# Kernel optimization log

Measured on AMD Instinct MI355X. Metric: run time of the kernel, lower is better.

The kernel has to match this reference:

```python
import jax, jax.numpy as jnp
import numpy as np

N_HEAD = 16
N_EMBD = 1024


def setup_inputs() -> dict:
    key = jax.random.key(0)
    k1, k2, k3 = jax.random.split(key, 3)
    B, T = 2, 2048
    x = jax.random.normal(k1, (B, T, N_EMBD), dtype=jnp.float32)
    w_attn = jax.random.normal(k2, (N_EMBD, 3 * N_EMBD), dtype=jnp.float32) * 0.02
    b_attn = jnp.zeros((3 * N_EMBD,), dtype=jnp.float32)
    w_proj = jax.random.normal(k3, (N_EMBD, N_EMBD), dtype=jnp.float32) * 0.02
    b_proj = jnp.zeros((N_EMBD,), dtype=jnp.float32)
    return {"x": x, "w_attn": w_attn, "b_attn": b_attn, "w_proj": w_proj, "b_proj": b_proj}


def _split_heads(t):
    # [B, T, E] -> [B, H, T, hd]
    B, T, E = t.shape
    return t.reshape(B, T, N_HEAD, E // N_HEAD).transpose(0, 2, 1, 3)


def reference(x, w_attn, b_attn, w_proj, b_proj):
    B, T, E = x.shape
    hd = E // N_HEAD
    c = x @ w_attn + b_attn                       # [B, T, 3E]
    q, k, v = jnp.split(c, 3, axis=2)
    q, k, v = _split_heads(q), _split_heads(k), _split_heads(v)  # [B,H,T,hd]
    present = jnp.stack((k, v), axis=1)           # [B, 2, H, T, hd]
    # scores, scaled by rsqrt(head_dim)
    w = jnp.einsum("bhqd,bhkd->bhqk", q, k) * jax.lax.rsqrt(jnp.float32(hd))
    # causal mask: w * mask + -1e9 * (1 - mask)  (faithful to the source)
    mask = jnp.tril(jnp.ones((T, T), dtype=w.dtype))[None, None]
    w = w * mask + (-1e9) * (1.0 - mask)
    w = jax.nn.softmax(w, axis=-1)
    a = jnp.einsum("bhqk,bhkd->bhqd", w, v)       # [B,H,T,hd]
    a = a.transpose(0, 2, 1, 3).reshape(B, T, E)  # merge heads
    a = a @ w_proj + b_proj
    return a, present
```

## Files before the change

kernel.cpp:

```cpp
#include <hip/hip_runtime.h>

typedef unsigned short u16b;
typedef __attribute__((ext_vector_type(4))) float f32x4;
typedef __attribute__((ext_vector_type(8))) short bf16x8;

#define GLD_LDS(g, l) __builtin_amdgcn_global_load_lds( \
    (__attribute__((address_space(1))) void*)(g), \
    (__attribute__((address_space(3))) void*)(l), 16, 0, 0)

__device__ __forceinline__ u16b f2bf(float f) {
    unsigned u = __builtin_bit_cast(unsigned, f);
    u += 0x7fffu + ((u >> 16) & 1u);
    return (u16b)(u >> 16);
}
__device__ __forceinline__ unsigned trunc_bf(float f) {
    return __builtin_bit_cast(unsigned, f) >> 16;
}

__global__ void cvt_f32_bf16(const float* __restrict__ in, u16b* __restrict__ out, int n4) {
    int i = blockIdx.x * blockDim.x + threadIdx.x;
    if (i < n4) {
        float4 v = ((const float4*)in)[i];
        uint2 o;
        o.x = (unsigned)f2bf(v.x) | ((unsigned)f2bf(v.y) << 16);
        o.y = (unsigned)f2bf(v.z) | ((unsigned)f2bf(v.w) << 16);
        ((uint2*)out)[i] = o;
    }
}

__global__ void transcvt(const float* __restrict__ in, u16b* __restrict__ out, int K, int N) {
    __shared__ float tile[32][33];
    int kt = blockIdx.x * 32, nt = blockIdx.y * 32;
    int c = threadIdx.x & 31, r8 = threadIdx.x >> 5;
    for (int i = 0; i < 4; i++) {
        int r = r8 + i * 8;
        tile[r][c] = in[(size_t)(kt + r) * N + nt + c];
    }
    __syncthreads();
    for (int i = 0; i < 4; i++) {
        int r = r8 + i * 8;
        out[(size_t)(nt + r) * K + kt + c] = f2bf(tile[c][r]);
    }
}

__global__ void trans_v(const u16b* __restrict__ in, u16b* __restrict__ out) {
    __shared__ u16b tile[64][66];
    const int bh = blockIdx.y;
    const int t0 = blockIdx.x * 64;
    const u16b* ip = in + (size_t)bh * 2048 * 64 + (size_t)t0 * 64;
    u16b* op = out + (size_t)bh * 64 * 2048 + t0;
    const int c = threadIdx.x & 7, r = threadIdx.x >> 3;
    #pragma unroll
    for (int it = 0; it < 2; it++) {
        int row = it * 32 + r;
        uint4 v = *(const uint4*)(ip + row * 64 + c * 8);
        const u16b* pv = (const u16b*)&v;
        #pragma unroll
        for (int e = 0; e < 8; e++) tile[c * 8 + e][row] = pv[e];
    }
    __syncthreads();
    const int d = threadIdx.x >> 2, c2 = threadIdx.x & 3;
    uint4 o[2];
    u16b* po = (u16b*)o;
    #pragma unroll
    for (int k = 0; k < 16; k++) po[k] = tile[d][c2 * 16 + k];
    *(uint4*)(op + d * 2048 + c2 * 16) = o[0];
    *(uint4*)(op + d * 2048 + c2 * 16 + 8) = o[1];
}

template<int EPI>
__global__ __launch_bounds__(256, 2) void gemm_bt(
    const u16b* __restrict__ A, const u16b* __restrict__ Bt,
    int M, int N, int K,
    const float* __restrict__ bias,
    float* __restrict__ out_f,
    u16b* __restrict__ q_ws, u16b* __restrict__ k_ws, u16b* __restrict__ v_ws)
{
    __shared__ u16b sA[128 * 64];
    __shared__ u16b sB[128 * 64];
    const int tid = threadIdx.x;
    const int l = tid & 63, w = tid >> 6;
    const int lr = l & 15, lg = l >> 4;
    const int m0 = blockIdx.y * 128, n0 = blockIdx.x * 128;
    const int wm = (w >> 1) * 64, wn = (w & 1) * 64;
    f32x4 acc[4][4] = {};

    for (int kt = 0; kt < K; kt += 64) {
        #pragma unroll
        for (int i = 0; i < 4; i++) {
            int chunk = i * 256 + tid;
            int row = chunk >> 3;
            int cb = (chunk & 7) ^ (row & 7);
            GLD_LDS(A + (size_t)(m0 + row) * K + kt + cb * 8, &sA[(i * 256 + w * 64) * 8]);
            GLD_LDS(Bt + (size_t)(n0 + row) * K + kt + cb * 8, &sB[(i * 256 + w * 64) * 8]);
        }
        __syncthreads();
        #pragma unroll
        for (int ks = 0; ks < 2; ks++) {
            bf16x8 af[4], bf[4];
            #pragma unroll
            for (int i = 0; i < 4; i++) {
                int arow = wm + i * 16 + lr;
                af[i] = *(const bf16x8*)((const char*)sA + arow * 128 + ((ks * 64 + lg * 16) ^ ((arow & 7) << 4)));
                int brow = wn + i * 16 + lr;
                bf[i] = *(const bf16x8*)((const char*)sB + brow * 128 + ((ks * 64 + lg * 16) ^ ((brow & 7) << 4)));
            }
            #pragma unroll
            for (int mi = 0; mi < 4; mi++)
                #pragma unroll
                for (int ni = 0; ni < 4; ni++)
                    acc[mi][ni] = __builtin_amdgcn_mfma_f32_16x16x32_bf16(af[mi], bf[ni], acc[mi][ni], 0, 0, 0);
        }
        __syncthreads();
    }

    if (EPI == 1) {
        #pragma unroll
        for (int ni = 0; ni < 4; ni++) {
            int col = n0 + wn + ni * 16 + lr;
            float bv = bias[col];
            #pragma unroll
            for (int mi = 0; mi < 4; mi++)
                #pragma unroll
                for (int jj = 0; jj < 4; jj++) {
                    int rowm = m0 + wm + mi * 16 + lg * 4 + jj;
                    out_f[(size_t)rowm * N + col] = acc[mi][ni][jj] + bv;
                }
        }
    } else {
        const int qkv = n0 >> 10;
        #pragma unroll
        for (int ni = 0; ni < 4; ni++) {
            int n = n0 + wn + ni * 16 + lr;
            float bv = bias[n];
            int h = (n >> 6) & 15, d = n & 63;
            #pragma unroll
            for (int mi = 0; mi < 4; mi++)
                #pragma unroll
                for (int jj = 0; jj < 4; jj++) {
                    int m = m0 + wm + mi * 16 + lg * 4 + jj;
                    int b = m >> 11, t = m & 2047;
                    float c = acc[mi][ni][jj] + bv;
                    size_t bhtd = ((size_t)(b * 16 + h) * 2048 + t) * 64 + d;
                    if (qkv == 0) {
                        q_ws[bhtd] = f2bf(c * 0.18033688011f);
                    } else if (qkv == 1) {
                        out_f[((size_t)((b * 2 + 0) * 16 + h) * 2048 + t) * 64 + d] = c;
                        k_ws[bhtd] = f2bf(c);
                    } else {
                        out_f[((size_t)((b * 2 + 1) * 16 + h) * 2048 + t) * 64 + d] = c;
                        v_ws[bhtd] = f2bf(c);
                    }
                }
        }
    }
}

__global__ __launch_bounds__(256, 4) void attn_fwd(
    const u16b* __restrict__ q_ws, const u16b* __restrict__ k_ws,
    const u16b* __restrict__ v_t, u16b* __restrict__ a_ws)
{
    __shared__ u16b sK[2][64 * 64];
    __shared__ u16b sV[2][64 * 64];
    __shared__ u16b sP[4][16 * 64];
    const int tid = threadIdx.x;
    const int l = tid & 63, w = tid >> 6;
    const int lr = l & 15, lg = l >> 4;
    const int g = blockIdx.x >> 5, bh = blockIdx.x & 31;
    const int a = g & 7, bq = g >> 3;
    const int qt = (bq == 0) ? a : (bq == 1) ? 15 - a : (bq == 2) ? 16 + a : 31 - a;
    const int b = bh >> 4, h = bh & 15;
    const size_t kbase = (size_t)bh * 2048 * 64;
    const size_t vbase = (size_t)bh * 64 * 2048;

    const int chunk0 = tid, chunk1 = 256 + tid;
    const int row0 = chunk0 >> 3, cb0 = (chunk0 & 7) ^ (row0 & 7);
    const int row1 = chunk1 >> 3, cb1 = (chunk1 & 7) ^ (row1 & 7);
    const u16b* kp0 = k_ws + kbase + (size_t)row0 * 64 + cb0 * 8;
    const u16b* kp1 = k_ws + kbase + (size_t)row1 * 64 + cb1 * 8;
    const u16b* vp0 = v_t + vbase + (size_t)row0 * 2048 + cb0 * 8;
    const u16b* vp1 = v_t + vbase + (size_t)row1 * 2048 + cb1 * 8;

    bf16x8 qf[2];
    {
        const u16b* qp = q_ws + kbase + (size_t)(qt * 64 + w * 16 + lr) * 64 + lg * 8;
        qf[0] = *(const bf16x8*)qp;
        qf[1] = *(const bf16x8*)(qp + 32);
    }
    const bf16x8 ones = {0x3F80, 0x3F80, 0x3F80, 0x3F80, 0x3F80, 0x3F80, 0x3F80, 0x3F80};
    f32x4 Oacc[4] = {};
    f32x4 Lacc = {};

    GLD_LDS(kp0, &sK[0][chunk0 * 8]);
    GLD_LDS(kp1, &sK[0][chunk1 * 8]);
    GLD_LDS(vp0, &sV[0][chunk0 * 8]);
    GLD_LDS(vp1, &sV[0][chunk1 * 8]);
    __syncthreads();
    int cur = 0;

    #pragma unroll 1
    for (int j = 0; j <= qt; j++) {
        if (j < qt) {
            int nxt = cur ^ 1;
            size_t ko = (size_t)(j + 1) * 64 * 64;
            size_t vo = (size_t)(j + 1) * 64;
            GLD_LDS(kp0 + ko, &sK[nxt][chunk0 * 8]);
            GLD_LDS(kp1 + ko, &sK[nxt][chunk1 * 8]);
            GLD_LDS(vp0 + vo, &sV[nxt][chunk0 * 8]);
            GLD_LDS(vp1 + vo, &sV[nxt][chunk1 * 8]);
        }
        const u16b* cK = &sK[cur][0];
        const u16b* cV = &sV[cur][0];

        f32x4 S[4];
        __builtin_amdgcn_s_setprio(1);
        #pragma unroll
        for (int c = 0; c < 4; c++) {
            f32x4 s = {};
            #pragma unroll
            for (int ks = 0; ks < 2; ks++) {
                int krow = c * 16 + lr;
                bf16x8 kf = *(const bf16x8*)((const char*)cK + krow * 128 + ((ks * 64 + lg * 16) ^ ((krow & 7) << 4)));
                s = __builtin_amdgcn_mfma_f32_16x16x32_bf16(kf, qf[ks], s, 0, 0, 0);
            }
            S[c] = s;
        }
        __builtin_amdgcn_s_setprio(0);
        if (j == qt) {
            const int ql = w * 16 + lr;
            #pragma unroll
            for (int c = 0; c < 4; c++)
                #pragma unroll
                for (int jj = 0; jj < 4; jj++)
                    if (c * 16 + lg * 4 + jj > ql) S[c][jj] = -1e9f;
        }
        u16b* myP = &sP[w][0];
        #pragma unroll
        for (int c = 0; c < 4; c++) {
            #pragma unroll
            for (int jj = 0; jj < 4; jj++)
                S[c][jj] = __builtin_amdgcn_exp2f(S[c][jj]);
            uint2 pk;
            pk.x = trunc_bf(S[c][0]) | (trunc_bf(S[c][1]) << 16);
            pk.y = trunc_bf(S[c][2]) | (trunc_bf(S[c][3]) << 16);
            *(uint2*)((char*)myP + lr * 128 + ((c * 32 + lg * 8) ^ ((lr & 7) << 4))) = pk;
        }
        __builtin_amdgcn_s_setprio(1);
        #pragma unroll
        for (int ks = 0; ks < 2; ks++) {
            bf16x8 pa = *(const bf16x8*)((const char*)myP + lr * 128 + ((ks * 64 + lg * 16) ^ ((lr & 7) << 4)));
            #pragma unroll
            for (int dc = 0; dc < 4; dc++) {
                int vrow = dc * 16 + lr;
                bf16x8 vb = *(const bf16x8*)((const char*)cV + vrow * 128 + ((ks * 64 + lg * 16) ^ ((vrow & 7) << 4)));
                Oacc[dc] = __builtin_amdgcn_mfma_f32_16x16x32_bf16(pa, vb, Oacc[dc], 0, 0, 0);
            }
            Lacc = __builtin_amdgcn_mfma_f32_16x16x32_bf16(pa, ones, Lacc, 0, 0, 0);
        }
        __builtin_amdgcn_s_setprio(0);
        __syncthreads();
        cur ^= 1;
    }
    #pragma unroll
    for (int jj = 0; jj < 4; jj++) {
        float inv = 1.f / Lacc[jj];
        int q = qt * 64 + w * 16 + lg * 4 + jj;
        #pragma unroll
        for (int dc = 0; dc < 4; dc++) {
            int d = dc * 16 + lr;
            a_ws[(size_t)(b * 2048 + q) * 1024 + h * 64 + d] = f2bf(Oacc[dc][jj] * inv);
        }
    }
}

extern "C" void kernel_launch(void* const* d_in, const int* in_sizes, int n_in,
                              void* d_out, int out_size, void* d_ws, size_t ws_size,
                              hipStream_t stream) {
    const float* x      = (const float*)d_in[0];
    const float* w_attn = (const float*)d_in[1];
    const float* b_attn = (const float*)d_in[2];
    const float* w_proj = (const float*)d_in[3];
    const float* b_proj = (const float*)d_in[4];
    float* out = (float*)d_out;
    float* present = out + 4194304;

    char* ws = (char*)d_ws;
    u16b* xb   = (u16b*)(ws);
    u16b* wab  = (u16b*)(ws + 8388608);
    u16b* wpb  = (u16b*)(ws + 14680064);
    u16b* q_ws = (u16b*)(ws + 16777216);
    u16b* k_ws = (u16b*)(ws + 25165824);
    u16b* v_ws = (u16b*)(ws + 33554432);
    u16b* a_ws = (u16b*)(ws + 41943040);
    u16b* v_t  = xb;

    cvt_f32_bf16<<<4096, 256, 0, stream>>>(x, xb, 1048576);
    transcvt<<<dim3(32, 96), 256, 0, stream>>>(w_attn, wab, 1024, 3072);
    transcvt<<<dim3(32, 32), 256, 0, stream>>>(w_proj, wpb, 1024, 1024);
    gemm_bt<0><<<dim3(24, 32), 256, 0, stream>>>(xb, wab, 4096, 3072, 1024, b_attn,
                                                 present, q_ws, k_ws, v_ws);
    trans_v<<<dim3(32, 32), 256, 0, stream>>>(v_ws, v_t);
    attn_fwd<<<1024, 256, 0, stream>>>(q_ws, k_ws, v_t, a_ws);
    gemm_bt<1><<<dim3(8, 32), 256, 0, stream>>>(a_ws, wpb, 4096, 1024, 1024, b_proj,
                                                out, nullptr, nullptr, nullptr);
}
```

Before: 117.8 us.

## Double-buffer GEMM LDS tiles, swizzle block order across XCDs, raise MFMA priority

```diff
diff --git a/kernel.cpp b/kernel.cpp
--- a/kernel.cpp
+++ b/kernel.cpp
@@ -76,43 +76,66 @@
     float* __restrict__ out_f,
     u16b* __restrict__ q_ws, u16b* __restrict__ k_ws, u16b* __restrict__ v_ws)
 {
-    __shared__ u16b sA[128 * 64];
-    __shared__ u16b sB[128 * 64];
+    __shared__ u16b sA[2][128 * 64];
+    __shared__ u16b sB[2][128 * 64];
     const int tid = threadIdx.x;
     const int l = tid & 63, w = tid >> 6;
     const int lr = l & 15, lg = l >> 4;
-    const int m0 = blockIdx.y * 128, n0 = blockIdx.x * 128;
+    const int nbx = N >> 7;
+    const int chunk = gridDim.x >> 3;
+    const int swz = (blockIdx.x & 7) * chunk + (blockIdx.x >> 3);
+    const int m0 = (swz / nbx) * 128, n0 = (swz % nbx) * 128;
     const int wm = (w >> 1) * 64, wn = (w & 1) * 64;
     f32x4 acc[4][4] = {};
 
+    int srow[4], scb[4];
+    #pragma unroll
+    for (int i = 0; i < 4; i++) {
+        int chk = i * 256 + tid;
+        srow[i] = chk >> 3;
+        scb[i] = (chk & 7) ^ (srow[i] & 7);
+    }
+
+#define STAGE_G(buf, kt)                                                          \
+    {                                                                             \
+        _Pragma("unroll")                                                         \
+        for (int i = 0; i < 4; i++) {                                             \
+            GLD_LDS(A + (size_t)(m0 + srow[i]) * K + (kt) + scb[i] * 8,           \
+                    &sA[buf][(i * 256 + w * 64) * 8]);                            \
+            GLD_LDS(Bt + (size_t)(n0 + srow[i]) * K + (kt) + scb[i] * 8,          \
+                    &sB[buf][(i * 256 + w * 64) * 8]);                            \
+        }                                                                         \
+    }
+
+    STAGE_G(0, 0);
+    __syncthreads();
+    int cur = 0;
+
+    #pragma unroll 1
     for (int kt = 0; kt < K; kt += 64) {
-        #pragma unroll
-        for (int i = 0; i < 4; i++) {
-            int chunk = i * 256 + tid;
-            int row = chunk >> 3;
-            int cb = (chunk & 7) ^ (row & 7);
-            GLD_LDS(A + (size_t)(m0 + row) * K + kt + cb * 8, &sA[(i * 256 + w * 64) * 8]);
-            GLD_LDS(Bt + (size_t)(n0 + row) * K + kt + cb * 8, &sB[(i * 256 + w * 64) * 8]);
-        }
-        __syncthreads();
+        if (kt + 64 < K) STAGE_G(cur ^ 1, kt + 64);
         #pragma unroll
         for (int ks = 0; ks < 2; ks++) {
             bf16x8 af[4], bf[4];
             #pragma unroll
             for (int i = 0; i < 4; i++) {
                 int arow = wm + i * 16 + lr;
-                af[i] = *(const bf16x8*)((const char*)sA + arow * 128 + ((ks * 64 + lg * 16) ^ ((arow & 7) << 4)));
+                af[i] = *(const bf16x8*)((const char*)&sA[cur][0] + arow * 128 + ((ks * 64 + lg * 16) ^ ((arow & 7) << 4)));
                 int brow = wn + i * 16 + lr;
-                bf[i] = *(const bf16x8*)((const char*)sB + brow * 128 + ((ks * 64 + lg * 16) ^ ((brow & 7) << 4)));
+                bf[i] = *(const bf16x8*)((const char*)&sB[cur][0] + brow * 128 + ((ks * 64 + lg * 16) ^ ((brow & 7) << 4)));
             }
+            __builtin_amdgcn_s_setprio(1);
             #pragma unroll
             for (int mi = 0; mi < 4; mi++)
                 #pragma unroll
                 for (int ni = 0; ni < 4; ni++)
                     acc[mi][ni] = __builtin_amdgcn_mfma_f32_16x16x32_bf16(af[mi], bf[ni], acc[mi][ni], 0, 0, 0);
+            __builtin_amdgcn_s_setprio(0);
         }
         __syncthreads();
-    }
+        cur ^= 1;
+    }
+#undef STAGE_G
 
     if (EPI == 1) {
         #pragma unroll
@@ -297,10 +320,10 @@
     cvt_f32_bf16<<<4096, 256, 0, stream>>>(x, xb, 1048576);
     transcvt<<<dim3(32, 96), 256, 0, stream>>>(w_attn, wab, 1024, 3072);
     transcvt<<<dim3(32, 32), 256, 0, stream>>>(w_proj, wpb, 1024, 1024);
-    gemm_bt<0><<<dim3(24, 32), 256, 0, stream>>>(xb, wab, 4096, 3072, 1024, b_attn,
-                                                 present, q_ws, k_ws, v_ws);
+    gemm_bt<0><<<768, 256, 0, stream>>>(xb, wab, 4096, 3072, 1024, b_attn,
+                                        present, q_ws, k_ws, v_ws);
     trans_v<<<dim3(32, 32), 256, 0, stream>>>(v_ws, v_t);
     attn_fwd<<<1024, 256, 0, stream>>>(q_ws, k_ws, v_t, a_ws);
-    gemm_bt<1><<<dim3(8, 32), 256, 0, stream>>>(a_ws, wpb, 4096, 1024, 1024, b_proj,
-                                                out, nullptr, nullptr, nullptr);
-}
+    gemm_bt<1><<<256, 256, 0, stream>>>(a_ws, wpb, 4096, 1024, 1024, b_proj,
+                                        out, nullptr, nullptr, nullptr);
+}
```

New measurement: 124.9 us. 6.1% more time.
